# Kernel tuning notes

Measured on AMD Instinct MI355X. Metric: run time of the kernel, lower is better.

The kernel has to match this reference:

```python
import jax, jax.numpy as jnp
import numpy as np

D1, K, B, C, T = 270, 32, 128, 273, 1024
KAIMING_BOUND = 1.0 / 32.0  # sqrt(6/((1+5)*K*K)) for a=sqrt(5), fan_in=K*K=1024


def setup_inputs() -> dict:
    key = jax.random.key(0)
    k1, k2, k3, k4 = jax.random.split(key, 4)
    X = jax.random.normal(k1, (B, C, T), dtype=jnp.float32)
    loc = jax.random.uniform(k2, (C, 2), dtype=jnp.float32)  # normalized 2D sensor coords
    z_re = jax.random.uniform(k3, (D1, K, K), minval=-KAIMING_BOUND, maxval=KAIMING_BOUND, dtype=jnp.float32)
    z_im = jax.random.uniform(k4, (D1, K, K), minval=-KAIMING_BOUND, maxval=KAIMING_BOUND, dtype=jnp.float32)
    return {"X": X, "loc": loc, "z_re": z_re, "z_im": z_im}


def reference(X, loc, z_re, z_im):
    # Algebraic rewrite of the D1*K*K python loop:
    # a[j,c] = sum_{k,l} z_re[j,k,l]*cos(2pi(k*x_c + l*y_c)) + z_im[j,k,l]*sin(...)
    x, y = loc[:, 0], loc[:, 1]                    # [C]
    k = jnp.arange(K, dtype=loc.dtype)
    phase = 2.0 * jnp.pi * (k[:, None, None] * x[None, None, :]
                            + k[None, :, None] * y[None, None, :])  # [K, K, C]
    a = (jnp.einsum('jkl,klc->jc', z_re, jnp.cos(phase))
         + jnp.einsum('jkl,klc->jc', z_im, jnp.sin(phase)))          # [D1, C]
    e = jnp.exp(a)
    w = e / jnp.sum(e, axis=1, keepdims=True)      # exp-normalized channel weights
    # out[b,j,t] = sum_c w[j,c] * X[b,c,t]  (stack over j + permute(1,0,2) in original)
    return jnp.einsum('jc,bct->bjt', w, X)
```

## Files before the change

### kernel.cpp

```cpp
#include <hip/hip_runtime.h>
#include <hip/hip_bf16.h>

#define NUM_D1 270
#define NUM_B  128
#define NUM_C  273
#define NUM_T  1024
#define KL     1024
#define TW     320
#define CP     288
#define CW     296
#define ROWB   (CW * 2)

#define WT_BYTES (144 * ROWB)
#define XB_BYTES (64 * ROWB)
#define LDS3_TOTAL (WT_BYTES + 2 * XB_BYTES)

typedef float f32x4 __attribute__((ext_vector_type(4)));
typedef __bf16 bf16x8 __attribute__((ext_vector_type(8)));
typedef unsigned short u16x8 __attribute__((ext_vector_type(8)));

static __device__ __forceinline__ unsigned short f2bf(float f) {
  unsigned u = __float_as_uint(f);
  unsigned r = (u + 0x7fffu + ((u >> 16) & 1u)) >> 16;
  return (unsigned short)r;
}

__global__ __launch_bounds__(256) void k_trig(const float* __restrict__ loc,
                                              float* __restrict__ cosT,
                                              float* __restrict__ sinT) {
  int idx = blockIdx.x * 256 + threadIdx.x;
  int kl = idx / TW;
  int c  = idx - kl * TW;
  float cv = 0.f, sv = 0.f;
  if (c < NUM_C) {
    float x = loc[2 * c], y = loc[2 * c + 1];
    float kf = (float)(kl >> 5), lf = (float)(kl & 31);
    float ph = 6.283185307179586f * (kf * x + lf * y);
    sincosf(ph, &sv, &cv);
  }
  cosT[idx] = cv;
  sinT[idx] = sv;
}

__global__ __launch_bounds__(1024) void k_agemm(const float* __restrict__ z_re,
                                                const float* __restrict__ z_im,
                                                const float* __restrict__ cosT,
                                                const float* __restrict__ sinT,
                                                float* __restrict__ a) {
  __shared__ float sm[4][8][64];
  int tid = threadIdx.x;
  int lane = tid & 63;
  int g = tid >> 6;
  int p = g >> 3;
  int q = g & 7;
  int jb = blockIdx.x;
  int cb = blockIdx.y;
  int c = cb * 64 + lane;
  int j_a = jb * 4 + p;
  int j_b = j_a + 2;
  int jeb = (j_b < NUM_D1) ? j_b : 0;
  const float* zr0 = z_re + (size_t)j_a * KL;
  const float* zi0 = z_im + (size_t)j_a * KL;
  const float* zr1 = z_re + (size_t)jeb * KL;
  const float* zi1 = z_im + (size_t)jeb * KL;
  float a0 = 0.f, a1 = 0.f;
  int k0 = q * 128;
  #pragma unroll 4
  for (int kk = k0; kk < k0 + 128; ++kk) {
    float cv = cosT[kk * TW + c];
    float sv = sinT[kk * TW + c];
    a0 = fmaf(zr0[kk], cv, a0);
    a0 = fmaf(zi0[kk], sv, a0);
    a1 = fmaf(zr1[kk], cv, a1);
    a1 = fmaf(zi1[kk], sv, a1);
  }
  sm[p][q][lane] = a0;
  sm[p + 2][q][lane] = a1;
  __syncthreads();
  if (tid < 256) {
    int jl = tid >> 6;
    int l2 = tid & 63;
    int j = jb * 4 + jl;
    int c2 = cb * 64 + l2;
    float s = 0.f;
    #pragma unroll
    for (int qq = 0; qq < 8; ++qq) s += sm[jl][qq][l2];
    if (j < NUM_D1 && c2 < NUM_C) a[j * CP + c2] = s;
  }
}

__global__ __launch_bounds__(256) void k_softmax(const float* __restrict__ a,
                                                 unsigned short* __restrict__ wg) {
  int wv = threadIdx.x >> 6;
  int lane = threadIdx.x & 63;
  int j = blockIdx.x * 4 + wv;
  if (j >= NUM_D1) {
    for (int c = lane; c < CW; c += 64) wg[j * CW + c] = 0;
    return;
  }
  float e[5];
  float s = 0.f;
  #pragma unroll
  for (int qq = 0; qq < 5; ++qq) {
    int c = qq * 64 + lane;
    float v = 0.f;
    if (c < NUM_C) v = expf(a[j * CP + c]);
    e[qq] = v;
    s += v;
  }
  #pragma unroll
  for (int o = 32; o > 0; o >>= 1) s += __shfl_xor(s, o, 64);
  float inv = 1.0f / s;
  #pragma unroll
  for (int qq = 0; qq < 5; ++qq) {
    int c = qq * 64 + lane;
    if (c < CW) wg[j * CW + c] = (c < NUM_C) ? f2bf(e[qq] * inv) : (unsigned short)0;
  }
}

__global__ __launch_bounds__(768) void k_out3(const float* __restrict__ X,
                                              const unsigned short* __restrict__ wg,
                                              float* __restrict__ out) {
  extern __shared__ char lds[];
  char* WTb = lds;
  char* XA  = lds + WT_BYTES;
  char* XBf = lds + WT_BYTES + XB_BYTES;

  const int tid = threadIdx.x;
  const int wv = tid >> 6, lane = tid & 63;
  const int rlo = lane & 15, kg = lane >> 4;
  const int jh = blockIdx.x;
  const int b  = blockIdx.y;
  const float* Xb = X + (size_t)b * (NUM_C * NUM_T);
  const int c8 = tid >> 4;
  const int t4 = tid & 15;
  const bool stg = (c8 < 36);

  f32x4 v[8];
  if (stg) {
    #pragma unroll
    for (int e = 0; e < 8; ++e) {
      int c = c8 * 8 + e;
      if (c < NUM_C) {
        v[e] = *(const f32x4*)(Xb + (size_t)c * NUM_T + t4 * 4);
      } else {
        v[e][0] = v[e][1] = v[e][2] = v[e][3] = 0.f;
      }
    }
  }
  {
    const char* wsrc = (const char*)wg + (size_t)jh * WT_BYTES;
    uint4 wv4[7];
    #pragma unroll
    for (int i = 0; i < 7; ++i) {
      int off = (tid + i * 768) * 16;
      if (off < WT_BYTES) wv4[i] = *(const uint4*)(wsrc + off);
    }
    #pragma unroll
    for (int i = 0; i < 7; ++i) {
      int off = (tid + i * 768) * 16;
      if (off < WT_BYTES) *(uint4*)(WTb + off) = wv4[i];
    }
  }
  if (stg) {
    #pragma unroll
    for (int f = 0; f < 4; ++f) {
      int tw = t4 * 4 + f;
      u16x8 pk;
      #pragma unroll
      for (int e = 0; e < 8; ++e) pk[e] = f2bf(v[e][f]);
      *(u16x8*)(XA + tw * ROWB + ((c8 * 16) ^ ((t4 & 3) << 4))) = pk;
    }
  }
  __syncthreads();

  const int tt = wv & 3, jq = wv >> 2;
  const int t = tt * 16 + rlo;
  const int sw = ((t >> 2) & 3) << 4;

  for (int it = 0; it < 16; ++it) {
    const int t0 = it * 64;
    char* xcur = (it & 1) ? XBf : XA;
    char* xnxt = (it & 1) ? XA : XBf;

    const bool pf = stg && (it < 15);
    if (pf) {
      #pragma unroll
      for (int e = 0; e < 8; ++e) {
        int c = c8 * 8 + e;
        if (c < NUM_C) {
          v[e] = *(const f32x4*)(Xb + (size_t)c * NUM_T + t0 + 64 + t4 * 4);
        } else {
          v[e][0] = v[e][1] = v[e][2] = v[e][3] = 0.f;
        }
      }
    }

    bf16x8 bfr[9];
    #pragma unroll
    for (int ks = 0; ks < 9; ++ks)
      bfr[ks] = *(const bf16x8*)(xcur + t * ROWB + ((ks * 64 + kg * 16) ^ sw));

    f32x4 acc[3];
    #pragma unroll
    for (int jt = 0; jt < 3; ++jt)
      acc[jt][0] = acc[jt][1] = acc[jt][2] = acc[jt][3] = 0.f;

    #pragma unroll
    for (int ks = 0; ks < 9; ++ks) {
      #pragma unroll
      for (int jt = 0; jt < 3; ++jt) {
        bf16x8 afr = *(const bf16x8*)(WTb +
            (size_t)((jq * 3 + jt) * 16 + rlo) * ROWB + kg * 16 + ks * 64);
        acc[jt] = __builtin_amdgcn_mfma_f32_16x16x32_bf16(afr, bfr[ks], acc[jt], 0, 0, 0);
      }
    }

    #pragma unroll
    for (int jt = 0; jt < 3; ++jt) {
      #pragma unroll
      for (int r = 0; r < 4; ++r) {
        int j = jh * 144 + (jq * 3 + jt) * 16 + kg * 4 + r;
        if (j < NUM_D1)
          __builtin_nontemporal_store(acc[jt][r],
              out + ((size_t)b * NUM_D1 + j) * NUM_T + t0 + t);
      }
    }

    if (it < 15) {
      if (pf) {
        #pragma unroll
        for (int f = 0; f < 4; ++f) {
          int tw = t4 * 4 + f;
          u16x8 pk;
          #pragma unroll
          for (int e = 0; e < 8; ++e) pk[e] = f2bf(v[e][f]);
          *(u16x8*)(xnxt + tw * ROWB + ((c8 * 16) ^ ((t4 & 3) << 4))) = pk;
        }
      }
      __syncthreads();
    }
  }
}

extern "C" void kernel_launch(void* const* d_in, const int* in_sizes, int n_in,
                              void* d_out, int out_size, void* d_ws, size_t ws_size,
                              hipStream_t stream) {
  const float* X   = (const float*)d_in[0];
  const float* loc = (const float*)d_in[1];
  const float* zre = (const float*)d_in[2];
  const float* zim = (const float*)d_in[3];
  float* out = (float*)d_out;
  char* ws = (char*)d_ws;
  float* cosT = (float*)(ws);
  float* sinT = (float*)(ws + 1310720);
  float* a    = (float*)(ws + 2621440);
  unsigned short* wgp = (unsigned short*)(ws + 2934784);

  (void)hipFuncSetAttribute((const void*)k_out3,
                            hipFuncAttributeMaxDynamicSharedMemorySize, LDS3_TOTAL);

  hipLaunchKernelGGL(k_trig,    dim3(1280),   dim3(256),  0, stream, loc, cosT, sinT);
  hipLaunchKernelGGL(k_agemm,   dim3(68, 5),  dim3(1024), 0, stream, zre, zim, cosT, sinT, a);
  hipLaunchKernelGGL(k_softmax, dim3(72),     dim3(256),  0, stream, a, wgp);
  hipLaunchKernelGGL(k_out3,    dim3(2, 128), dim3(768),  LDS3_TOTAL, stream, X, wgp, out);
}
```

Before: 132.6 us.

## Hold weight fragments in registers and drop LDS weight tile in output GEMM

```diff
diff --git a/kernel.cpp b/kernel.cpp
--- a/kernel.cpp
+++ b/kernel.cpp
@@ -11,13 +11,11 @@
 #define CW     296
 #define ROWB   (CW * 2)
 
-#define WT_BYTES (144 * ROWB)
 #define XB_BYTES (64 * ROWB)
-#define LDS3_TOTAL (WT_BYTES + 2 * XB_BYTES)
+#define LDS4_TOTAL (2 * XB_BYTES)
 
 typedef float f32x4 __attribute__((ext_vector_type(4)));
 typedef __bf16 bf16x8 __attribute__((ext_vector_type(8)));
-typedef unsigned short u16x8 __attribute__((ext_vector_type(8)));
 
 static __device__ __forceinline__ unsigned short f2bf(float f) {
   unsigned u = __float_as_uint(f);
@@ -118,13 +116,12 @@
   }
 }
 
-__global__ __launch_bounds__(768) void k_out3(const float* __restrict__ X,
-                                              const unsigned short* __restrict__ wg,
-                                              float* __restrict__ out) {
+__global__ __launch_bounds__(768, 3) void k_out4(const float* __restrict__ X,
+                                                 const unsigned short* __restrict__ wg,
+                                                 float* __restrict__ out) {
   extern __shared__ char lds[];
-  char* WTb = lds;
-  char* XA  = lds + WT_BYTES;
-  char* XBf = lds + WT_BYTES + XB_BYTES;
+  char* XA  = lds;
+  char* XBf = lds + XB_BYTES;
 
   const int tid = threadIdx.x;
   const int wv = tid >> 6, lane = tid & 63;
@@ -132,74 +129,77 @@
   const int jh = blockIdx.x;
   const int b  = blockIdx.y;
   const float* Xb = X + (size_t)b * (NUM_C * NUM_T);
-  const int c8 = tid >> 4;
+
+  const int co = tid >> 4;
   const int t4 = tid & 15;
-  const bool stg = (c8 < 36);
-
-  f32x4 v[8];
-  if (stg) {
-    #pragma unroll
-    for (int e = 0; e < 8; ++e) {
-      int c = c8 * 8 + e;
-      if (c < NUM_C) {
-        v[e] = *(const f32x4*)(Xb + (size_t)c * NUM_T + t4 * 4);
-      } else {
-        v[e][0] = v[e][1] = v[e][2] = v[e][3] = 0.f;
-      }
-    }
-  }
-  {
-    const char* wsrc = (const char*)wg + (size_t)jh * WT_BYTES;
-    uint4 wv4[7];
-    #pragma unroll
-    for (int i = 0; i < 7; ++i) {
-      int off = (tid + i * 768) * 16;
-      if (off < WT_BYTES) wv4[i] = *(const uint4*)(wsrc + off);
-    }
-    #pragma unroll
-    for (int i = 0; i < 7; ++i) {
-      int off = (tid + i * 768) * 16;
-      if (off < WT_BYTES) *(uint4*)(WTb + off) = wv4[i];
-    }
-  }
-  if (stg) {
-    #pragma unroll
-    for (int f = 0; f < 4; ++f) {
-      int tw = t4 * 4 + f;
-      u16x8 pk;
-      #pragma unroll
-      for (int e = 0; e < 8; ++e) pk[e] = f2bf(v[e][f]);
-      *(u16x8*)(XA + tw * ROWB + ((c8 * 16) ^ ((t4 & 3) << 4))) = pk;
-    }
-  }
-  __syncthreads();
+  const bool stg = (co < 36);
+  const int swz = (t4 & 3) << 4;
 
   const int tt = wv & 3, jq = wv >> 2;
   const int t = tt * 16 + rlo;
   const int sw = ((t >> 2) & 3) << 4;
+
+  f32x4 va[4], vb[4];
+  if (stg) {
+    #pragma unroll
+    for (int e = 0; e < 4; ++e) {
+      int c = co * 8 + e;
+      if (c < NUM_C) va[e] = *(const f32x4*)(Xb + (size_t)c * NUM_T + t4 * 4);
+      else { va[e][0] = va[e][1] = va[e][2] = va[e][3] = 0.f; }
+    }
+    #pragma unroll
+    for (int e = 0; e < 4; ++e) {
+      int c = co * 8 + 4 + e;
+      if (c < NUM_C) vb[e] = *(const f32x4*)(Xb + (size_t)c * NUM_T + t4 * 4);
+      else { vb[e][0] = vb[e][1] = vb[e][2] = vb[e][3] = 0.f; }
+    }
+  }
+
+  bf16x8 afr[3][9];
+  #pragma unroll
+  for (int jt = 0; jt < 3; ++jt) {
+    int row = jh * 144 + (jq * 3 + jt) * 16 + rlo;
+    const char* rp = (const char*)wg + (size_t)row * ROWB + kg * 16;
+    #pragma unroll
+    for (int ks = 0; ks < 9; ++ks)
+      afr[jt][ks] = *(const bf16x8*)(rp + ks * 64);
+  }
+
+  if (stg) {
+    char* rb = XA;
+    #pragma unroll
+    for (int f = 0; f < 4; ++f) {
+      int tw = t4 * 4 + f;
+      ushort4 pk;
+      pk.x = f2bf(va[0][f]); pk.y = f2bf(va[1][f]);
+      pk.z = f2bf(va[2][f]); pk.w = f2bf(va[3][f]);
+      *(ushort4*)(rb + tw * ROWB + ((co * 16) ^ swz)) = pk;
+    }
+    #pragma unroll
+    for (int f = 0; f < 4; ++f) {
+      int tw = t4 * 4 + f;
+      ushort4 pk;
+      pk.x = f2bf(vb[0][f]); pk.y = f2bf(vb[1][f]);
+      pk.z = f2bf(vb[2][f]); pk.w = f2bf(vb[3][f]);
+      *(ushort4*)(rb + tw * ROWB + ((co * 16 + 8) ^ swz)) = pk;
+    }
+  }
+  __syncthreads();
 
   for (int it = 0; it < 16; ++it) {
     const int t0 = it * 64;
     char* xcur = (it & 1) ? XBf : XA;
     char* xnxt = (it & 1) ? XA : XBf;
-
     const bool pf = stg && (it < 15);
+
     if (pf) {
       #pragma unroll
-      for (int e = 0; e < 8; ++e) {
-        int c = c8 * 8 + e;
-        if (c < NUM_C) {
-          v[e] = *(const f32x4*)(Xb + (size_t)c * NUM_T + t0 + 64 + t4 * 4);
-        } else {
-          v[e][0] = v[e][1] = v[e][2] = v[e][3] = 0.f;
-        }
-      }
-    }
-
-    bf16x8 bfr[9];
-    #pragma unroll
-    for (int ks = 0; ks < 9; ++ks)
-      bfr[ks] = *(const bf16x8*)(xcur + t * ROWB + ((ks * 64 + kg * 16) ^ sw));
+      for (int e = 0; e < 4; ++e) {
+        int c = co * 8 + e;
+        if (c < NUM_C) va[e] = *(const f32x4*)(Xb + (size_t)c * NUM_T + t0 + 64 + t4 * 4);
+        else { va[e][0] = va[e][1] = va[e][2] = va[e][3] = 0.f; }
+      }
+    }
 
     f32x4 acc[3];
     #pragma unroll
@@ -208,11 +208,18 @@
 
     #pragma unroll
     for (int ks = 0; ks < 9; ++ks) {
-      #pragma unroll
-      for (int jt = 0; jt < 3; ++jt) {
-        bf16x8 afr = *(const bf16x8*)(WTb +
-            (size_t)((jq * 3 + jt) * 16 + rlo) * ROWB + kg * 16 + ks * 64);
-        acc[jt] = __builtin_amdgcn_mfma_f32_16x16x32_bf16(afr, bfr[ks], acc[jt], 0, 0, 0);
+      bf16x8 bfr = *(const bf16x8*)(xcur + t * ROWB + ((ks * 64 + kg * 16) ^ sw));
+      #pragma unroll
+      for (int jt = 0; jt < 3; ++jt)
+        acc[jt] = __builtin_amdgcn_mfma_f32_16x16x32_bf16(afr[jt][ks], bfr, acc[jt], 0, 0, 0);
+    }
+
+    if (pf) {
+      #pragma unroll
+      for (int e = 0; e < 4; ++e) {
+        int c = co * 8 + 4 + e;
+        if (c < NUM_C) vb[e] = *(const f32x4*)(Xb + (size_t)c * NUM_T + t0 + 64 + t4 * 4);
+        else { vb[e][0] = vb[e][1] = vb[e][2] = vb[e][3] = 0.f; }
       }
     }
 
@@ -222,8 +229,7 @@
       for (int r = 0; r < 4; ++r) {
         int j = jh * 144 + (jq * 3 + jt) * 16 + kg * 4 + r;
         if (j < NUM_D1)
-          __builtin_nontemporal_store(acc[jt][r],
-              out + ((size_t)b * NUM_D1 + j) * NUM_T + t0 + t);
+          out[((size_t)b * NUM_D1 + j) * NUM_T + t0 + t] = acc[jt][r];
       }
     }
 
@@ -232,10 +238,18 @@
         #pragma unroll
         for (int f = 0; f < 4; ++f) {
           int tw = t4 * 4 + f;
-          u16x8 pk;
-          #pragma unroll
-          for (int e = 0; e < 8; ++e) pk[e] = f2bf(v[e][f]);
-          *(u16x8*)(xnxt + tw * ROWB + ((c8 * 16) ^ ((t4 & 3) << 4))) = pk;
+          ushort4 pk;
+          pk.x = f2bf(va[0][f]); pk.y = f2bf(va[1][f]);
+          pk.z = f2bf(va[2][f]); pk.w = f2bf(va[3][f]);
+          *(ushort4*)(xnxt + tw * ROWB + ((co * 16) ^ swz)) = pk;
+        }
+        #pragma unroll
+        for (int f = 0; f < 4; ++f) {
+          int tw = t4 * 4 + f;
+          ushort4 pk;
+          pk.x = f2bf(vb[0][f]); pk.y = f2bf(vb[1][f]);
+          pk.z = f2bf(vb[2][f]); pk.w = f2bf(vb[3][f]);
+          *(ushort4*)(xnxt + tw * ROWB + ((co * 16 + 8) ^ swz)) = pk;
         }
       }
       __syncthreads();
@@ -257,11 +271,11 @@
   float* a    = (float*)(ws + 2621440);
   unsigned short* wgp = (unsigned short*)(ws + 2934784);
 
-  (void)hipFuncSetAttribute((const void*)k_out3,
-                            hipFuncAttributeMaxDynamicSharedMemorySize, LDS3_TOTAL);
+  (void)hipFuncSetAttribute((const void*)k_out4,
+                            hipFuncAttributeMaxDynamicSharedMemorySize, LDS4_TOTAL);
 
   hipLaunchKernelGGL(k_trig,    dim3(1280),   dim3(256),  0, stream, loc, cosT, sinT);
   hipLaunchKernelGGL(k_agemm,   dim3(68, 5),  dim3(1024), 0, stream, zre, zim, cosT, sinT, a);
   hipLaunchKernelGGL(k_softmax, dim3(72),     dim3(256),  0, stream, a, wgp);
-  hipLaunchKernelGGL(k_out3,    dim3(2, 128), dim3(768),  LDS3_TOTAL, stream, X, wgp, out);
-}
+  hipLaunchKernelGGL(k_out4,    dim3(2, 128), dim3(768),  LDS4_TOTAL, stream, X, wgp, out);
+}
```

After: 227.7 us. +71.7%, slower.

## Remap output-GEMM blocks per XCD and hand-schedule prefetch waits and barriers

Applied to the files above, without the earlier changes.

```diff
diff --git a/kernel.cpp b/kernel.cpp
--- a/kernel.cpp
+++ b/kernel.cpp
@@ -13,11 +13,10 @@
 
 #define WT_BYTES (144 * ROWB)
 #define XB_BYTES (64 * ROWB)
-#define LDS3_TOTAL (WT_BYTES + 2 * XB_BYTES)
+#define LDS5_TOTAL (WT_BYTES + 2 * XB_BYTES)
 
 typedef float f32x4 __attribute__((ext_vector_type(4)));
 typedef __bf16 bf16x8 __attribute__((ext_vector_type(8)));
-typedef unsigned short u16x8 __attribute__((ext_vector_type(8)));
 
 static __device__ __forceinline__ unsigned short f2bf(float f) {
   unsigned u = __float_as_uint(f);
@@ -118,9 +117,9 @@
   }
 }
 
-__global__ __launch_bounds__(768) void k_out3(const float* __restrict__ X,
-                                              const unsigned short* __restrict__ wg,
-                                              float* __restrict__ out) {
+__global__ __launch_bounds__(768, 3) void k_out5(const float* __restrict__ X,
+                                                 const unsigned short* __restrict__ wg,
+                                                 float* __restrict__ out) {
   extern __shared__ char lds[];
   char* WTb = lds;
   char* XA  = lds + WT_BYTES;
@@ -129,77 +128,70 @@
   const int tid = threadIdx.x;
   const int wv = tid >> 6, lane = tid & 63;
   const int rlo = lane & 15, kg = lane >> 4;
-  const int jh = blockIdx.x;
-  const int b  = blockIdx.y;
+
+  const int lin = blockIdx.x;
+  const int xcd = lin & 7, slot = lin >> 3;
+  const int jh = slot & 1;
+  const int b  = xcd * 16 + (slot >> 1);
+
   const float* Xb = X + (size_t)b * (NUM_C * NUM_T);
-  const int c8 = tid >> 4;
+
+  const int co = tid >> 4;
   const int t4 = tid & 15;
-  const bool stg = (c8 < 36);
-
-  f32x4 v[8];
-  if (stg) {
-    #pragma unroll
-    for (int e = 0; e < 8; ++e) {
-      int c = c8 * 8 + e;
-      if (c < NUM_C) {
-        v[e] = *(const f32x4*)(Xb + (size_t)c * NUM_T + t4 * 4);
-      } else {
-        v[e][0] = v[e][1] = v[e][2] = v[e][3] = 0.f;
-      }
-    }
-  }
-  {
-    const char* wsrc = (const char*)wg + (size_t)jh * WT_BYTES;
-    uint4 wv4[7];
-    #pragma unroll
-    for (int i = 0; i < 7; ++i) {
-      int off = (tid + i * 768) * 16;
-      if (off < WT_BYTES) wv4[i] = *(const uint4*)(wsrc + off);
-    }
-    #pragma unroll
-    for (int i = 0; i < 7; ++i) {
-      int off = (tid + i * 768) * 16;
-      if (off < WT_BYTES) *(uint4*)(WTb + off) = wv4[i];
-    }
-  }
-  if (stg) {
-    #pragma unroll
-    for (int f = 0; f < 4; ++f) {
-      int tw = t4 * 4 + f;
-      u16x8 pk;
-      #pragma unroll
-      for (int e = 0; e < 8; ++e) pk[e] = f2bf(v[e][f]);
-      *(u16x8*)(XA + tw * ROWB + ((c8 * 16) ^ ((t4 & 3) << 4))) = pk;
-    }
-  }
-  __syncthreads();
+  const bool stg = (co < 36);
+  const int swz = (t4 & 3) << 4;
 
   const int tt = wv & 3, jq = wv >> 2;
   const int t = tt * 16 + rlo;
   const int sw = ((t >> 2) & 3) << 4;
+
+  f32x4 va[8];
+  if (stg) {
+    #pragma unroll
+    for (int e = 0; e < 8; ++e) {
+      int c = co * 8 + e;
+      if (c < NUM_C) va[e] = *(const f32x4*)(Xb + (size_t)c * NUM_T + t4 * 4);
+      else { va[e][0] = va[e][1] = va[e][2] = va[e][3] = 0.f; }
+    }
+  }
+  {
+    const char* wsrc = (const char*)wg + (size_t)jh * WT_BYTES;
+    #pragma unroll
+    for (int i = 0; i < 7; ++i) {
+      int off = (tid + i * 768) * 16;
+      if (off < WT_BYTES) *(uint4*)(WTb + off) = *(const uint4*)(wsrc + off);
+    }
+  }
+  if (stg) {
+    #pragma unroll
+    for (int f = 0; f < 4; ++f) {
+      int tw = t4 * 4 + f;
+      ushort4 p0, p1;
+      p0.x = f2bf(va[0][f]); p0.y = f2bf(va[1][f]);
+      p0.z = f2bf(va[2][f]); p0.w = f2bf(va[3][f]);
+      p1.x = f2bf(va[4][f]); p1.y = f2bf(va[5][f]);
+      p1.z = f2bf(va[6][f]); p1.w = f2bf(va[7][f]);
+      *(ushort4*)(XA + tw * ROWB + ((co * 16) ^ swz)) = p0;
+      *(ushort4*)(XA + tw * ROWB + ((co * 16 + 8) ^ swz)) = p1;
+    }
+  }
+  __syncthreads();
 
   for (int it = 0; it < 16; ++it) {
     const int t0 = it * 64;
     char* xcur = (it & 1) ? XBf : XA;
     char* xnxt = (it & 1) ? XA : XBf;
-
     const bool pf = stg && (it < 15);
+
     if (pf) {
       #pragma unroll
       for (int e = 0; e < 8; ++e) {
-        int c = c8 * 8 + e;
-        if (c < NUM_C) {
-          v[e] = *(const f32x4*)(Xb + (size_t)c * NUM_T + t0 + 64 + t4 * 4);
-        } else {
-          v[e][0] = v[e][1] = v[e][2] = v[e][3] = 0.f;
-        }
-      }
-    }
-
-    bf16x8 bfr[9];
-    #pragma unroll
-    for (int ks = 0; ks < 9; ++ks)
-      bfr[ks] = *(const bf16x8*)(xcur + t * ROWB + ((ks * 64 + kg * 16) ^ sw));
+        int c = co * 8 + e;
+        if (c < NUM_C) va[e] = *(const f32x4*)(Xb + (size_t)c * NUM_T + t0 + 64 + t4 * 4);
+        else { va[e][0] = va[e][1] = va[e][2] = va[e][3] = 0.f; }
+      }
+    }
+    __builtin_amdgcn_sched_barrier(0);
 
     f32x4 acc[3];
     #pragma unroll
@@ -208,11 +200,12 @@
 
     #pragma unroll
     for (int ks = 0; ks < 9; ++ks) {
+      bf16x8 bfr = *(const bf16x8*)(xcur + t * ROWB + ((ks * 64 + kg * 16) ^ sw));
       #pragma unroll
       for (int jt = 0; jt < 3; ++jt) {
         bf16x8 afr = *(const bf16x8*)(WTb +
             (size_t)((jq * 3 + jt) * 16 + rlo) * ROWB + kg * 16 + ks * 64);
-        acc[jt] = __builtin_amdgcn_mfma_f32_16x16x32_bf16(afr, bfr[ks], acc[jt], 0, 0, 0);
+        acc[jt] = __builtin_amdgcn_mfma_f32_16x16x32_bf16(afr, bfr, acc[jt], 0, 0, 0);
       }
     }
 
@@ -222,23 +215,30 @@
       for (int r = 0; r < 4; ++r) {
         int j = jh * 144 + (jq * 3 + jt) * 16 + kg * 4 + r;
         if (j < NUM_D1)
-          __builtin_nontemporal_store(acc[jt][r],
-              out + ((size_t)b * NUM_D1 + j) * NUM_T + t0 + t);
+          out[((size_t)b * NUM_D1 + j) * NUM_T + t0 + t] = acc[jt][r];
       }
     }
 
     if (it < 15) {
+      asm volatile("s_waitcnt vmcnt(12)" ::: "memory");
+      __builtin_amdgcn_sched_barrier(0);
       if (pf) {
         #pragma unroll
         for (int f = 0; f < 4; ++f) {
           int tw = t4 * 4 + f;
-          u16x8 pk;
-          #pragma unroll
-          for (int e = 0; e < 8; ++e) pk[e] = f2bf(v[e][f]);
-          *(u16x8*)(xnxt + tw * ROWB + ((c8 * 16) ^ ((t4 & 3) << 4))) = pk;
+          ushort4 p0, p1;
+          p0.x = f2bf(va[0][f]); p0.y = f2bf(va[1][f]);
+          p0.z = f2bf(va[2][f]); p0.w = f2bf(va[3][f]);
+          p1.x = f2bf(va[4][f]); p1.y = f2bf(va[5][f]);
+          p1.z = f2bf(va[6][f]); p1.w = f2bf(va[7][f]);
+          *(ushort4*)(xnxt + tw * ROWB + ((co * 16) ^ swz)) = p0;
+          *(ushort4*)(xnxt + tw * ROWB + ((co * 16 + 8) ^ swz)) = p1;
         }
       }
-      __syncthreads();
+      asm volatile("s_waitcnt lgkmcnt(0)" ::: "memory");
+      __builtin_amdgcn_sched_barrier(0);
+      __builtin_amdgcn_s_barrier();
+      __builtin_amdgcn_sched_barrier(0);
     }
   }
 }
@@ -257,11 +257,11 @@
   float* a    = (float*)(ws + 2621440);
   unsigned short* wgp = (unsigned short*)(ws + 2934784);
 
-  (void)hipFuncSetAttribute((const void*)k_out3,
-                            hipFuncAttributeMaxDynamicSharedMemorySize, LDS3_TOTAL);
+  (void)hipFuncSetAttribute((const void*)k_out5,
+                            hipFuncAttributeMaxDynamicSharedMemorySize, LDS5_TOTAL);
 
   hipLaunchKernelGGL(k_trig,    dim3(1280),   dim3(256),  0, stream, loc, cosT, sinT);
   hipLaunchKernelGGL(k_agemm,   dim3(68, 5),  dim3(1024), 0, stream, zre, zim, cosT, sinT, a);
   hipLaunchKernelGGL(k_softmax, dim3(72),     dim3(256),  0, stream, a, wgp);
-  hipLaunchKernelGGL(k_out3,    dim3(2, 128), dim3(768),  LDS3_TOTAL, stream, X, wgp, out);
-}
+  hipLaunchKernelGGL(k_out5,    dim3(256),    dim3(768),  LDS5_TOTAL, stream, X, wgp, out);
+}
```

Result: no change. 133.3 us (+0.5%).
